# Performance work log

Hardware: AMD Instinct MI355X
Metric: run time of the kernel (lower is better)

## Reference

```python
import jax, jax.numpy as jnp
import numpy as np

H_, W_, KNN, KO = 64, 64, 32, 32
TAU, ETA, LAMBDA0, ALPHA = 1.5, 8.0, 0.001, 10.0
A_, B_, BETA, BETA_P = 1.0, 0.0, 8.0, 8.0
SMOOTH_KS, SMOOTH_SIGMA, EPS = 5, 1.0, 1e-6


def _base_grid(h, w):
    ys = jnp.arange(h, dtype=jnp.float32)
    xs = jnp.arange(w, dtype=jnp.float32)
    yy, xx = jnp.meshgrid(ys, xs, indexing='ij')
    return jnp.stack([xx.reshape(-1), yy.reshape(-1)], axis=-1)  # (N,2) as (x,y)


def _offset_bins(K_o, h, w):
    maxr = (h ** 2 + w ** 2) ** 0.5 * 0.5
    ks = jnp.arange(1, K_o + 1, dtype=jnp.float32)
    angles = 2.0 * jnp.pi * (ks - 1) / K_o
    radii = 0.2 * maxr + 0.6 * maxr * (ks - 1) / (K_o - 1 + 1e-9)
    return jnp.stack([radii * jnp.cos(angles), radii * jnp.sin(angles)], axis=-1)  # (K_o,2)


def _gaussian_kernel(ks, sigma):
    ax = jnp.arange(-(ks // 2), ks // 2 + 1, dtype=jnp.float32)  # matches torch -ks//2+1 .. ks//2 for odd ks
    xx, yy = jnp.meshgrid(ax, ax, indexing='ij')
    k = jnp.exp(-(xx ** 2 + yy ** 2) / (2.0 * sigma ** 2))
    return (k / k.sum()).reshape(1, 1, ks, ks)


def setup_inputs() -> dict:
    key = jax.random.key(0)
    k1, k2 = jax.random.split(key)
    B, N = 2, H_ * W_
    E = jax.random.normal(k1, (B, N, 256), dtype=jnp.float32)
    A0 = jax.random.uniform(k2, (B, N, N), dtype=jnp.float32)
    return {
        'E': E,
        'A0': A0,
        'P': _base_grid(H_, W_),
        'bins': _offset_bins(KO, H_, W_),
        'smooth_kernel': _gaussian_kernel(SMOOTH_KS, SMOOTH_SIGMA),
    }


def reference(E, A0, P, bins, smooth_kernel):
    B, N, _ = A0.shape
    # top-k neighbors per row (sorted descending, like torch.topk)
    topk_vals, topk_idx = jax.lax.top_k(A0, KNN)  # (B,N,k)

    # offset vectors to neighbors
    p_j = P[topk_idx]                              # (B,N,k,2)
    v = p_j - P[None, :, None, :]                  # (B,N,k,2)
    diff = v[..., None, :] - bins[None, None, None, :, :]   # (B,N,k,K_o,2)
    dist2 = (diff ** 2).sum(-1)                    # (B,N,k,K_o)
    kappa = jnp.exp(-dist2 / (2.0 * TAU ** 2 + 1e-12))

    # global bin histogram and softmax weights
    Hbins = (topk_vals[..., None] * kappa).sum(axis=(1, 2))   # (B,K_o)
    Wsoft = jax.nn.softmax(ETA * Hbins, axis=-1)              # (B,K_o)

    R_edges = LAMBDA0 + (Wsoft[:, None, None, :] * kappa).sum(-1)  # (B,N,k)
    tildeA = topk_vals * R_edges
    A1_edges = tildeA / (tildeA.sum(-1, keepdims=True) + EPS)

    # entropy -> backgroundness U
    p = jax.nn.softmax(ALPHA * A1_edges, axis=-1)
    entropy = -(p * jnp.log(p + EPS)).sum(-1)      # (B,N)
    U = jax.nn.sigmoid(-A_ * entropy + B_)
    m = 1.0 - U

    # mask both endpoints of each edge
    m_j = jax.vmap(jnp.take)(m, topk_idx)          # (B,N,k)
    hatA = m[:, :, None] * A1_edges * m_j
    A2_edges = hatA / (hatA.sum(-1, keepdims=True) + EPS)

    # scatter sparse edges back to dense NxN (row indices unique per row)
    b_idx = jnp.arange(B)[:, None, None]
    n_idx = jnp.arange(N)[None, :, None]
    A2_dense = jnp.zeros((B, N, N), A2_edges.dtype).at[b_idx, n_idx, topk_idx].set(A2_edges)
    A2_dense = A2_dense / (A2_dense.sum(-1, keepdims=True) + EPS)

    # directional evidence
    exp_fwd = jnp.exp(BETA * A2_dense)
    exp_rev = jnp.swapaxes(exp_fwd, -1, -2)
    P_dir = exp_fwd / (exp_fwd + exp_rev + EPS)
    eye = jnp.eye(N, dtype=A2_dense.dtype)
    P_dir = P_dir * (1.0 - eye)                    # zero diagonal
    s_ev = (A2_dense * P_dir).sum(-1)
    A2_T = jnp.swapaxes(A2_dense, -1, -2)
    t_ev = (A2_T * (1.0 - jnp.swapaxes(P_dir, -1, -2))).sum(-1)
    pi_src = s_ev / (s_ev + t_ev + EPS)
    pi_tgt = 1.0 - pi_src

    # spatial attention map
    W_mean = Wsoft.mean(0)                         # (K_o,)
    chi = (kappa * W_mean[None, None, None, :]).sum(-1)       # (B,N,k)
    w_local = jax.nn.softmax(BETA_P * A2_edges, axis=-1)
    q = (w_local * chi).sum(-1)                    # (B,N)
    A1_map = q.reshape(B, 1, H_, W_)
    pad = SMOOTH_KS // 2
    smoothed = jax.lax.conv_general_dilated(A1_map, smooth_kernel, (1, 1), [(pad, pad), (pad, pad)])
    A1_map = jax.nn.sigmoid(smoothed)              # (B,1,h,w)

    return (A2_dense, U, pi_src, pi_tgt, A1_map)
```

## Files before the change

### kernel.cpp

```cpp
#include <hip/hip_runtime.h>
#include <math.h>

#define NN 4096
#define KK 32
#define KOb 32
#define BB 2
#define NSLOT 64

constexpr float EPS = 1e-6f;

typedef float nfloat4 __attribute__((ext_vector_type(4)));

#define WS_VALS   0
#define WS_IDX    (WS_VALS + BB*NN*KK)
#define WS_HBP    (WS_IDX + BB*NN*KK)
#define WS_TBL    (WS_HBP + BB*NSLOT*KOb)
#define WS_A1     (WS_TBL + BB*KOb*4)
#define WS_M      (WS_A1 + BB*NN*KK)
#define WS_CHI    (WS_M + BB*NN)
#define WS_A2     (WS_CHI + BB*NN*KK)
#define WS_SEV    (WS_A2 + BB*NN*KK)
#define WS_TEV    (WS_SEV + BB*NN)
#define WS_Q      (WS_TEV + BB*NN)

#define OUT_A2   0
#define OUT_U    ((size_t)BB*NN*NN)
#define OUT_PSRC (OUT_U + BB*NN)
#define OUT_PTGT (OUT_PSRC + BB*NN)
#define OUT_MAP  (OUT_PTGT + BB*NN)

__device__ __forceinline__ unsigned int fkey(float x) {
    unsigned int u = __float_as_uint(x);
    return u ^ ((unsigned int)((int)u >> 31) | 0x80000000u);
}
__device__ __forceinline__ float key2f(unsigned int k) {
    unsigned int u = (k & 0x80000000u) ? (k ^ 0x80000000u) : ~k;
    return __uint_as_float(u);
}

__global__ __launch_bounds__(256) void k_topk(const float* __restrict__ A0,
                                              const float* __restrict__ bins,
                                              float* __restrict__ ws) {
    __shared__ float sbins[2 * KOb];
    __shared__ int   scnt[2][4];
    __shared__ int   swtot[4];
    __shared__ unsigned long long cand[64];
    __shared__ float selv[KK], seldx[KK], seldy[KK];
    __shared__ float shb[KOb];

    const int t = threadIdx.x;
    const int wv = t >> 6, lane = t & 63;
    const int R = blockIdx.x;
    const int b = R >> 12;
    const int r = R & (NN - 1);

    if (t < 2 * KOb) sbins[t] = bins[t];
    if (t < KOb) shb[t] = 0.f;

    const nfloat4* row4 = (const nfloat4*)(A0 + (size_t)R * NN);
    unsigned int key[16];
    #pragma unroll
    for (int i = 0; i < 4; ++i) {
        const nfloat4 f = __builtin_nontemporal_load(row4 + i * 256 + t);
        key[4 * i + 0] = fkey(f.x);
        key[4 * i + 1] = fkey(f.y);
        key[4 * i + 2] = fkey(f.z);
        key[4 * i + 3] = fkey(f.w);
    }

    unsigned int lo = 0u, hi = 0xFFFFFFFFu;
    int cnt = NN, it = 0;
    while (cnt > 64) {
        unsigned int mid;
        if (it == 0)      mid = 0xBF7E0000u;
        else if (it == 1) mid = 0xBF7C4000u;
        else              mid = lo + ((hi - lo) >> 1);
        if (mid <= lo || mid >= hi) mid = lo + ((hi - lo) >> 1);
        if (mid == lo) break;
        int cl = 0;
        #pragma unroll
        for (int j = 0; j < 16; ++j) cl += (key[j] > mid) ? 1 : 0;
        int c = cl;
        #pragma unroll
        for (int m = 32; m >= 1; m >>= 1) c += __shfl_xor(c, m);
        const int p = it & 1;
        if (lane == 0) scnt[p][wv] = c;
        __syncthreads();
        const int ctot = scnt[p][0] + scnt[p][1] + scnt[p][2] + scnt[p][3];
        if (ctot >= KK) { lo = mid; cnt = ctot; } else hi = mid;
        if (++it > 48) break;
    }

    int cl = 0;
    #pragma unroll
    for (int j = 0; j < 16; ++j) cl += (key[j] > lo) ? 1 : 0;
    int inc = cl;
    #pragma unroll
    for (int m = 1; m < 64; m <<= 1) {
        const int o = __shfl_up(inc, m);
        if (lane >= m) inc += o;
    }
    if (lane == 63) swtot[wv] = inc;
    __syncthreads();
    int off = inc - cl;
    #pragma unroll
    for (int w = 0; w < 4; ++w) if (w < wv) off += swtot[w];
    const int nc0 = swtot[0] + swtot[1] + swtot[2] + swtot[3];
    const int ncand = (nc0 < 64) ? nc0 : 64;

    int slot = off;
    #pragma unroll
    for (int j = 0; j < 16; ++j) {
        if (key[j] > lo && slot < 64) {
            const unsigned int gidx = (unsigned int)((j >> 2) * 1024 + t * 4 + (j & 3));
            cand[slot] = ((unsigned long long)key[j] << 32)
                       | (unsigned long long)(4095u - gidx);
            ++slot;
        }
    }
    __syncthreads();

    if (t < 64) {
        const unsigned long long cd = (t < ncand) ? cand[t] : 0ull;
        int rank = 0;
        #pragma unroll
        for (int i = 0; i < 64; ++i) {
            const unsigned long long o = __shfl(cd, i);
            rank += (o > cd) ? 1 : 0;
        }
        if (t < ncand && rank < KK) {
            const float val = key2f((unsigned int)(cd >> 32));
            const int gidx = 4095 - (int)(cd & 0xFFFull);
            ws[WS_VALS + (size_t)R * KK + rank] = val;
            ((int*)(ws + WS_IDX))[(size_t)R * KK + rank] = gidx;
            selv[rank]  = val;
            seldx[rank] = (float)((gidx & 63) - (r & 63));
            seldy[rank] = (float)((gidx >> 6) - (r >> 6));
        }
    }
    __syncthreads();

    const int e = t >> 3;
    const float v = selv[e], dx0 = seldx[e], dy0 = seldy[e];
    #pragma unroll
    for (int jj = 0; jj < 4; ++jj) {
        const int o = (lane & 7) * 4 + jj;
        const float dx = dx0 - sbins[2 * o], dy = dy0 - sbins[2 * o + 1];
        float contrib = v * __expf(-(dx * dx + dy * dy) * (1.0f / 4.5f));
        contrib += __shfl_xor(contrib, 8);
        contrib += __shfl_xor(contrib, 16);
        contrib += __shfl_xor(contrib, 32);
        if ((lane >> 3) == 0) atomicAdd(&shb[o], contrib);
    }
    __syncthreads();
    if (t < KOb)
        atomicAdd(ws + WS_HBP + b * (NSLOT * KOb) + (R & (NSLOT - 1)) * KOb + t,
                  shb[t]);
}

__global__ __launch_bounds__(256) void k_hb(const float* __restrict__ bins,
                                            float* __restrict__ ws) {
    __shared__ float sred[64];
    const int t = threadIdx.x;
    if (t < 64) sred[t] = 0.f;
    __syncthreads();
    {
        const int p = t & 63, g = t >> 6;
        const int bb = p >> 5, oo = p & 31;
        float sum = 0.f;
        #pragma unroll
        for (int s = 0; s < 16; ++s)
            sum += ws[WS_HBP + bb * (NSLOT * KOb) + (g * 16 + s) * KOb + oo];
        atomicAdd(&sred[p], sum);
    }
    __syncthreads();
    if (t < 64) {
        const int oo = t & 31;
        const float h = 8.0f * sred[t];
        float mx = h;
        #pragma unroll
        for (int m = 16; m >= 1; m >>= 1) mx = fmaxf(mx, __shfl_xor(mx, m));
        const float e2 = __expf(h - mx);
        float ss = e2;
        #pragma unroll
        for (int m = 16; m >= 1; m >>= 1) ss += __shfl_xor(ss, m);
        const float wsf = e2 / ss;
        const float wm = 0.5f * (wsf + __shfl_xor(wsf, 32));
        ((float4*)(ws + WS_TBL))[t] =
            make_float4(bins[2 * oo], bins[2 * oo + 1], wsf, wm);
    }
}

__global__ __launch_bounds__(256) void k_row1(float* __restrict__ ws,
                                              float* __restrict__ out_u) {
    __shared__ float4 stbl[BB * KOb];
    const int t = threadIdx.x;
    if (t < BB * KOb) stbl[t] = ((const float4*)(ws + WS_TBL))[t];
    __syncthreads();

    const int wv = t >> 6, lane = t & 63;
    const int half = lane >> 5, k = lane & 31;
    const int R = blockIdx.x * 8 + wv * 2 + half;
    const int b = R >> 12;
    const int r = R & (NN - 1);

    const float val = ws[WS_VALS + (size_t)R * KK + k];
    const int c = ((int*)(ws + WS_IDX))[(size_t)R * KK + k];
    const float dx0 = (float)((c & 63) - (r & 63));
    const float dy0 = (float)((c >> 6) - (r >> 6));
    float racc = 0.f, cacc = 0.f;
    const float4* tb = stbl + (b << 5);
    #pragma unroll
    for (int o = 0; o < KOb; ++o) {
        const float4 cb = tb[o];
        const float dx = dx0 - cb.x, dy = dy0 - cb.y;
        const float kap = __expf(-(dx * dx + dy * dy) * (1.0f / 4.5f));
        racc += cb.z * kap;
        cacc += cb.w * kap;
    }
    const float Redge = 0.001f + racc;
    const float chi = cacc;

    const float tilde = val * Redge;
    float s = tilde;
    #pragma unroll
    for (int m = 16; m >= 1; m >>= 1) s += __shfl_xor(s, m);
    const float a1 = tilde / (s + EPS);

    const float z = 10.f * a1;
    float mz = z;
    #pragma unroll
    for (int m = 16; m >= 1; m >>= 1) mz = fmaxf(mz, __shfl_xor(mz, m));
    const float e = __expf(z - mz);
    float se = e;
    #pragma unroll
    for (int m = 16; m >= 1; m >>= 1) se += __shfl_xor(se, m);
    const float p = e / se;
    const float ent_t = -p * __logf(p + EPS);
    float ent = ent_t;
    #pragma unroll
    for (int m = 16; m >= 1; m >>= 1) ent += __shfl_xor(ent, m);
    const float U = 1.f / (1.f + __expf(ent));

    ws[WS_A1  + (size_t)R * KK + k] = a1;
    ws[WS_CHI + (size_t)R * KK + k] = chi;
    if (k == 0) { out_u[R] = U; ws[WS_M + R] = 1.f - U; }
}

__global__ __launch_bounds__(256) void k_row2d(float* __restrict__ ws,
                                               float* __restrict__ outA2) {
    __shared__ float srow[NN];
    const int R = blockIdx.x;
    const int b = R >> 12;
    const int t = threadIdx.x;

    const int gid = blockIdx.x * 256 + t;
    if (gid < BB * NN) ws[WS_TEV + gid] = 0.f;

    nfloat4* s4 = (nfloat4*)srow;
    const nfloat4 z4 = {0.f, 0.f, 0.f, 0.f};
    #pragma unroll
    for (int i = 0; i < 4; ++i) s4[t + 256 * i] = z4;

    float dvr = 0.f; int cr = -1;
    if (t < 64) {
        const int lane = t;
        const bool act = lane < 32;
        const int k = lane;
        const float mi = ws[WS_M + R];
        float a1 = 0.f; int c = 0; float mj = 0.f;
        if (act) {
            a1 = ws[WS_A1 + (size_t)R * KK + k];
            c = ((int*)(ws + WS_IDX))[(size_t)R * KK + k];
            mj = ws[WS_M + b * NN + c];
        }
        const float hat = act ? mi * a1 * mj : 0.f;
        float S = hat;
        #pragma unroll
        for (int m = 16; m >= 1; m >>= 1) S += __shfl_xor(S, m);
        const float a2e = hat / (S + EPS);
        float S2 = a2e;
        #pragma unroll
        for (int m = 16; m >= 1; m >>= 1) S2 += __shfl_xor(S2, m);
        const float dv = a2e / (S2 + EPS);

        const float z = act ? 8.f * a2e : -1e30f;
        float mz = z;
        #pragma unroll
        for (int m = 16; m >= 1; m >>= 1) mz = fmaxf(mz, __shfl_xor(mz, m));
        const float e = act ? __expf(z - mz) : 0.f;
        float se = e;
        #pragma unroll
        for (int m = 16; m >= 1; m >>= 1) se += __shfl_xor(se, m);
        const float wl = e / se;
        const float chi = act ? ws[WS_CHI + (size_t)R * KK + k] : 0.f;
        float q = act ? wl * chi : 0.f;
        #pragma unroll
        for (int m = 16; m >= 1; m >>= 1) q += __shfl_xor(q, m);
        if (lane == 0) ws[WS_Q + R] = q;

        if (act) {
            ws[WS_A2 + (size_t)R * KK + k] = dv;
            dvr = dv; cr = c;
        }
    }
    __syncthreads();
    if (cr >= 0) srow[cr] = dvr;
    __syncthreads();
    nfloat4* o4 = (nfloat4*)(outA2 + (size_t)R * NN);
    #pragma unroll
    for (int i = 0; i < 4; ++i)
        __builtin_nontemporal_store(s4[t + 256 * i], o4 + t + 256 * i);
}

__global__ __launch_bounds__(256) void k_dir(float* __restrict__ ws) {
    const int t = threadIdx.x;
    const int wv = t >> 6, lane = t & 63;
    const int half = lane >> 5, k = lane & 31;
    const int R = blockIdx.x * 8 + wv * 2 + half;
    const int b = R >> 12;
    const int r = R & (NN - 1);

    const float a = ws[WS_A2 + (size_t)R * KK + k];
    const int c = ((int*)(ws + WS_IDX))[(size_t)R * KK + k];
    float pdir = 0.f;
    if (c != r) {
        const int4* irow = (const int4*)((const int*)(ws + WS_IDX)
                                         + (size_t)(b * NN + c) * KK);
        int p = -1;
        #pragma unroll
        for (int q = 0; q < 8; ++q) {
            const int4 i4 = irow[q];
            if (i4.x == r) p = q * 4 + 0;
            if (i4.y == r) p = q * 4 + 1;
            if (i4.z == r) p = q * 4 + 2;
            if (i4.w == r) p = q * 4 + 3;
        }
        const float arev = (p >= 0) ? ws[WS_A2 + (size_t)(b * NN + c) * KK + p] : 0.f;
        const float ef = __expf(8.f * a), er = __expf(8.f * arev);
        pdir = ef / (ef + er + EPS);
    }
    float s = a * pdir;
    #pragma unroll
    for (int m = 16; m >= 1; m >>= 1) s += __shfl_xor(s, m);
    if (k == 0) ws[WS_SEV + R] = s;
    atomicAdd(ws + WS_TEV + b * NN + c, a * (1.f - pdir));
}

__global__ void k_tail(const float* __restrict__ ws, const float* __restrict__ kern,
                       float* __restrict__ out_psrc, float* __restrict__ out_ptgt,
                       float* __restrict__ out_map) {
    const int i = blockIdx.x * 256 + threadIdx.x;
    const float s = ws[WS_SEV + i], tv = ws[WS_TEV + i];
    const float ps = s / (s + tv + EPS);
    out_psrc[i] = ps;
    out_ptgt[i] = 1.f - ps;

    const int b = i >> 12;
    const int pix = i & 4095;
    const int y = pix >> 6, x = pix & 63;
    float acc = 0.f;
    #pragma unroll
    for (int ky = 0; ky < 5; ++ky) {
        const int yy = y + ky - 2;
        if (yy < 0 || yy >= 64) continue;
        #pragma unroll
        for (int kx = 0; kx < 5; ++kx) {
            const int xx = x + kx - 2;
            if (xx < 0 || xx >= 64) continue;
            acc += ws[WS_Q + b * 4096 + yy * 64 + xx] * kern[ky * 5 + kx];
        }
    }
    out_map[i] = 1.f / (1.f + __expf(-acc));
}

extern "C" void kernel_launch(void* const* d_in, const int* in_sizes, int n_in,
                              void* d_out, int out_size, void* d_ws, size_t ws_size,
                              hipStream_t stream) {
    const float* A0   = (const float*)d_in[1];
    const float* bins = (const float*)d_in[3];
    const float* kern = (const float*)d_in[4];
    float* out = (float*)d_out;
    float* ws  = (float*)d_ws;

    (void)hipMemsetAsync(ws + WS_HBP, 0, BB * NSLOT * KOb * sizeof(float), stream);

    k_topk <<<BB * NN,       256, 0, stream>>>(A0, bins, ws);
    k_hb   <<<1,             256, 0, stream>>>(bins, ws);
    k_row1 <<<BB * NN / 8,   256, 0, stream>>>(ws, out + OUT_U);
    k_row2d<<<BB * NN,       256, 0, stream>>>(ws, out);
    k_dir  <<<BB * NN / 8,   256, 0, stream>>>(ws);
    k_tail <<<BB * NN / 256, 256, 0, stream>>>(ws, kern,
                                               out + OUT_PSRC, out + OUT_PTGT,
                                               out + OUT_MAP);
}
```

Baseline: 286.5 us.

## Move dense A2 row writes into the directional kernel and pack row2 eight rows per block

The per-row normalisation and local-softmax stage now runs as a compact kernel that handles eight rows per block, with no dense output writes. The dense A2 row scatter and store is folded into the directional-evidence kernel, which already has each row's values and indices. This replaces two kernels, one lightweight and one heavy one-row-per-block, with one lightweight and one heavy. The cost is that the heavy one-block-per-row kernel now also does the reverse-index search and atomics on a single wave, which may lengthen it.

```diff
diff --git a/kernel.cpp b/kernel.cpp
--- a/kernel.cpp
+++ b/kernel.cpp
@@ -247,104 +247,98 @@
     if (k == 0) { out_u[R] = U; ws[WS_M + R] = 1.f - U; }
 }
 
-__global__ __launch_bounds__(256) void k_row2d(float* __restrict__ ws,
-                                               float* __restrict__ outA2) {
-    __shared__ float srow[NN];
-    const int R = blockIdx.x;
-    const int b = R >> 12;
-    const int t = threadIdx.x;
-
+__global__ __launch_bounds__(256) void k_row2m(float* __restrict__ ws) {
+    const int t = threadIdx.x;
     const int gid = blockIdx.x * 256 + t;
     if (gid < BB * NN) ws[WS_TEV + gid] = 0.f;
 
-    nfloat4* s4 = (nfloat4*)srow;
-    const nfloat4 z4 = {0.f, 0.f, 0.f, 0.f};
-    #pragma unroll
-    for (int i = 0; i < 4; ++i) s4[t + 256 * i] = z4;
-
-    float dvr = 0.f; int cr = -1;
-    if (t < 64) {
-        const int lane = t;
-        const bool act = lane < 32;
-        const int k = lane;
-        const float mi = ws[WS_M + R];
-        float a1 = 0.f; int c = 0; float mj = 0.f;
-        if (act) {
-            a1 = ws[WS_A1 + (size_t)R * KK + k];
-            c = ((int*)(ws + WS_IDX))[(size_t)R * KK + k];
-            mj = ws[WS_M + b * NN + c];
-        }
-        const float hat = act ? mi * a1 * mj : 0.f;
-        float S = hat;
-        #pragma unroll
-        for (int m = 16; m >= 1; m >>= 1) S += __shfl_xor(S, m);
-        const float a2e = hat / (S + EPS);
-        float S2 = a2e;
-        #pragma unroll
-        for (int m = 16; m >= 1; m >>= 1) S2 += __shfl_xor(S2, m);
-        const float dv = a2e / (S2 + EPS);
-
-        const float z = act ? 8.f * a2e : -1e30f;
-        float mz = z;
-        #pragma unroll
-        for (int m = 16; m >= 1; m >>= 1) mz = fmaxf(mz, __shfl_xor(mz, m));
-        const float e = act ? __expf(z - mz) : 0.f;
-        float se = e;
-        #pragma unroll
-        for (int m = 16; m >= 1; m >>= 1) se += __shfl_xor(se, m);
-        const float wl = e / se;
-        const float chi = act ? ws[WS_CHI + (size_t)R * KK + k] : 0.f;
-        float q = act ? wl * chi : 0.f;
-        #pragma unroll
-        for (int m = 16; m >= 1; m >>= 1) q += __shfl_xor(q, m);
-        if (lane == 0) ws[WS_Q + R] = q;
-
-        if (act) {
-            ws[WS_A2 + (size_t)R * KK + k] = dv;
-            dvr = dv; cr = c;
-        }
-    }
-    __syncthreads();
-    if (cr >= 0) srow[cr] = dvr;
-    __syncthreads();
-    nfloat4* o4 = (nfloat4*)(outA2 + (size_t)R * NN);
-    #pragma unroll
-    for (int i = 0; i < 4; ++i)
-        __builtin_nontemporal_store(s4[t + 256 * i], o4 + t + 256 * i);
-}
-
-__global__ __launch_bounds__(256) void k_dir(float* __restrict__ ws) {
-    const int t = threadIdx.x;
     const int wv = t >> 6, lane = t & 63;
     const int half = lane >> 5, k = lane & 31;
     const int R = blockIdx.x * 8 + wv * 2 + half;
     const int b = R >> 12;
+
+    const float mi = ws[WS_M + R];
+    const float a1 = ws[WS_A1 + (size_t)R * KK + k];
+    const int c = ((int*)(ws + WS_IDX))[(size_t)R * KK + k];
+    const float mj = ws[WS_M + b * NN + c];
+
+    const float hat = mi * a1 * mj;
+    float S = hat;
+    #pragma unroll
+    for (int m = 16; m >= 1; m >>= 1) S += __shfl_xor(S, m);
+    const float a2e = hat / (S + EPS);
+    float S2 = a2e;
+    #pragma unroll
+    for (int m = 16; m >= 1; m >>= 1) S2 += __shfl_xor(S2, m);
+    const float dv = a2e / (S2 + EPS);
+
+    const float z = 8.f * a2e;
+    float mz = z;
+    #pragma unroll
+    for (int m = 16; m >= 1; m >>= 1) mz = fmaxf(mz, __shfl_xor(mz, m));
+    const float e = __expf(z - mz);
+    float se = e;
+    #pragma unroll
+    for (int m = 16; m >= 1; m >>= 1) se += __shfl_xor(se, m);
+    const float wl = e / se;
+    const float chi = ws[WS_CHI + (size_t)R * KK + k];
+    float q = wl * chi;
+    #pragma unroll
+    for (int m = 16; m >= 1; m >>= 1) q += __shfl_xor(q, m);
+
+    ws[WS_A2 + (size_t)R * KK + k] = dv;
+    if (k == 0) ws[WS_Q + R] = q;
+}
+
+__global__ __launch_bounds__(256) void k_dirw(float* __restrict__ ws,
+                                              float* __restrict__ outA2) {
+    __shared__ float srow[NN];
+    const int R = blockIdx.x;
+    const int b = R >> 12;
     const int r = R & (NN - 1);
-
-    const float a = ws[WS_A2 + (size_t)R * KK + k];
-    const int c = ((int*)(ws + WS_IDX))[(size_t)R * KK + k];
-    float pdir = 0.f;
-    if (c != r) {
-        const int4* irow = (const int4*)((const int*)(ws + WS_IDX)
-                                         + (size_t)(b * NN + c) * KK);
-        int p = -1;
-        #pragma unroll
-        for (int q = 0; q < 8; ++q) {
-            const int4 i4 = irow[q];
-            if (i4.x == r) p = q * 4 + 0;
-            if (i4.y == r) p = q * 4 + 1;
-            if (i4.z == r) p = q * 4 + 2;
-            if (i4.w == r) p = q * 4 + 3;
-        }
-        const float arev = (p >= 0) ? ws[WS_A2 + (size_t)(b * NN + c) * KK + p] : 0.f;
-        const float ef = __expf(8.f * a), er = __expf(8.f * arev);
-        pdir = ef / (ef + er + EPS);
-    }
-    float s = a * pdir;
-    #pragma unroll
-    for (int m = 16; m >= 1; m >>= 1) s += __shfl_xor(s, m);
-    if (k == 0) ws[WS_SEV + R] = s;
-    atomicAdd(ws + WS_TEV + b * NN + c, a * (1.f - pdir));
+    const int t = threadIdx.x;
+
+    nfloat4* s4 = (nfloat4*)srow;
+    const nfloat4 z4 = {0.f, 0.f, 0.f, 0.f};
+    #pragma unroll
+    for (int i = 0; i < 4; ++i) s4[t + 256 * i] = z4;
+
+    float dvr = 0.f; int cr = -1;
+    if (t < 32) {
+        const int k = t;
+        const float a = ws[WS_A2 + (size_t)R * KK + k];
+        const int c = ((int*)(ws + WS_IDX))[(size_t)R * KK + k];
+        float pdir = 0.f;
+        if (c != r) {
+            const int4* irow = (const int4*)((const int*)(ws + WS_IDX)
+                                             + (size_t)(b * NN + c) * KK);
+            int p = -1;
+            #pragma unroll
+            for (int q = 0; q < 8; ++q) {
+                const int4 i4 = irow[q];
+                if (i4.x == r) p = q * 4 + 0;
+                if (i4.y == r) p = q * 4 + 1;
+                if (i4.z == r) p = q * 4 + 2;
+                if (i4.w == r) p = q * 4 + 3;
+            }
+            const float arev = (p >= 0) ? ws[WS_A2 + (size_t)(b * NN + c) * KK + p] : 0.f;
+            const float ef = __expf(8.f * a), er = __expf(8.f * arev);
+            pdir = ef / (ef + er + EPS);
+        }
+        float s = a * pdir;
+        #pragma unroll
+        for (int m = 16; m >= 1; m >>= 1) s += __shfl_xor(s, m);
+        if (k == 0) ws[WS_SEV + R] = s;
+        atomicAdd(ws + WS_TEV + b * NN + c, a * (1.f - pdir));
+        dvr = a; cr = c;
+    }
+    __syncthreads();
+    if (cr >= 0) srow[cr] = dvr;
+    __syncthreads();
+    nfloat4* o4 = (nfloat4*)(outA2 + (size_t)R * NN);
+    #pragma unroll
+    for (int i = 0; i < 4; ++i)
+        __builtin_nontemporal_store(s4[t + 256 * i], o4 + t + 256 * i);
 }
 
 __global__ void k_tail(const float* __restrict__ ws, const float* __restrict__ kern,
@@ -388,8 +382,8 @@
     k_topk <<<BB * NN,       256, 0, stream>>>(A0, bins, ws);
     k_hb   <<<1,             256, 0, stream>>>(bins, ws);
     k_row1 <<<BB * NN / 8,   256, 0, stream>>>(ws, out + OUT_U);
-    k_row2d<<<BB * NN,       256, 0, stream>>>(ws, out);
-    k_dir  <<<BB * NN / 8,   256, 0, stream>>>(ws);
+    k_row2m<<<BB * NN / 8,   256, 0, stream>>>(ws);
+    k_dirw <<<BB * NN,       256, 0, stream>>>(ws, out);
     k_tail <<<BB * NN / 256, 256, 0, stream>>>(ws, kern,
                                                out + OUT_PSRC, out + OUT_PTGT,
                                                out + OUT_MAP);
```

Result: faster. 275.5 us, median of 2 (-3.8%).
